# Kernel tuning notes

Hardware: AMD Instinct MI355X
Metric: run time of the kernel (lower is better)

The kernel has to match this reference:

```python
import jax, jax.numpy as jnp
import numpy as np

N_NODES = 100000
N_EDGES = 1600000
N_KEEP = 1280000  # int(N_EDGES * (1 - thr_a)), thr_a = 0.2
F_IN = 128
F_OUT = 128


def setup_inputs() -> dict:
    key = jax.random.key(0)
    ks = jax.random.split(key, 7)
    x = jax.random.normal(ks[0], (N_NODES, F_IN), dtype=jnp.float32)
    W = jax.random.normal(ks[1], (F_OUT, F_IN), dtype=jnp.float32) * (1.0 / np.sqrt(F_IN))
    bias = jax.random.normal(ks[2], (F_OUT,), dtype=jnp.float32)
    edge_src = jax.random.randint(ks[3], (N_EDGES,), 0, N_NODES, dtype=jnp.int32)
    edge_dst = jax.random.randint(ks[4], (N_EDGES,), 0, N_NODES, dtype=jnp.int32)
    edge_weight = jax.random.uniform(ks[5], (N_EDGES,), dtype=jnp.float32)
    idx_keep = jax.random.randint(ks[6], (N_KEEP,), 0, N_EDGES, dtype=jnp.int32)
    return {"x": x, "W": W, "bias": bias, "edge_src": edge_src,
            "edge_dst": edge_dst, "edge_weight": edge_weight, "idx_keep": idx_keep}


def reference(x, W, bias, edge_src, edge_dst, edge_weight, idx_keep):
    # Linear transform (pyg GCNConv lin has bias=False): h = x @ W.T  -> [N, F_out]
    h = jnp.einsum('nf,of->no', x, W)
    # Edge pruning: keep a random subset of edges (scheme_a='keep')
    src = edge_src[idx_keep]          # [M_keep]
    dst = edge_dst[idx_keep]          # [M_keep]
    ew = edge_weight[idx_keep]        # [M_keep]
    # propagate: message_j = h[src] * ew ; scatter-add into dst
    msg = h[src] * ew[:, None]        # [M_keep, F_out]
    out = jax.ops.segment_sum(msg, dst, num_segments=N_NODES)
    # GCNConv separate bias
    out = out + bias
    return out
```

## Files before the change

### kernel.cpp

```cpp
#include <hip/hip_runtime.h>

#define F 128
#define LDS_STRIDE 136
#define BUCKET 40

#define NPART 64
#define PCAP 22000
#define BIN_CAP 80
#define BIN_STRIDE 81
#define PA_CHUNK 2048
#define PB_CHUNK 1024
#define PB_CHUNKS 22

typedef __attribute__((ext_vector_type(8))) short short8;
typedef __attribute__((ext_vector_type(4))) float floatx4;
typedef __attribute__((ext_vector_type(4))) float f32x4;

__device__ __forceinline__ unsigned short f32_to_bf16(float x) {
    unsigned u = __float_as_uint(x);
    unsigned r = u + 0x7FFFu + ((u >> 16) & 1u);
    return (unsigned short)(r >> 16);
}


__global__ __launch_bounds__(256, 2) void gemm_and_partition(
    const float4* __restrict__ x4, const float4* __restrict__ W4,
    unsigned short* __restrict__ h2,
    int* __restrict__ cnt, int n_nodes,
    const int* __restrict__ idx_keep, const int* __restrict__ edge_dst,
    unsigned* __restrict__ pair_buf, int* __restrict__ pair_cnt,
    int m, int npp, int n_gemm_tiles, int n_part_chunks)
{
    __shared__ __align__(16) char smem[2 * 128 * LDS_STRIDE * 2];
    const int tid = threadIdx.x;
    const int bid = blockIdx.x;

    for (int i = bid * 256 + tid; i < n_nodes; i += gridDim.x * 256)
        cnt[i] = 0;

    const int r = bid % 9, c = bid / 9;

    if (r < 5) {
        const int tile = c * 5 + r;
        if (tile >= n_gemm_tiles) return;
        short* xs  = (short*)smem;
        short* wls = xs + 128 * LDS_STRIDE;
        const int node0 = tile * 128;

        for (int i = tid; i < 128 * 32; i += 256) {
            int row = i >> 5, c4 = i & 31;
            float4 v = W4[i];
            ushort4 b;
            b.x = f32_to_bf16(v.x); b.y = f32_to_bf16(v.y);
            b.z = f32_to_bf16(v.z); b.w = f32_to_bf16(v.w);
            *(ushort4*)&wls[row * LDS_STRIDE + c4 * 4] = b;
        }
        for (int i = tid; i < 128 * 32; i += 256) {
            int row = i >> 5, c4 = i & 31;
            int n = node0 + row;
            f32x4 v = (n < n_nodes)
                          ? __builtin_nontemporal_load((const f32x4*)&x4[(size_t)n * 32 + c4])
                          : (f32x4){0.f, 0.f, 0.f, 0.f};
            ushort4 b;
            b.x = f32_to_bf16(v[0]); b.y = f32_to_bf16(v[1]);
            b.z = f32_to_bf16(v[2]); b.w = f32_to_bf16(v[3]);
            *(ushort4*)&xs[row * LDS_STRIDE + c4 * 4] = b;
        }
        __syncthreads();

        const int wave = tid >> 6, lane = tid & 63;
        const int row16 = lane & 15, quad = lane >> 4;
        const int wrow0 = wave * 32;

        floatx4 acc[2][8];
        #pragma unroll
        for (int rr = 0; rr < 2; ++rr)
            #pragma unroll
            for (int cc = 0; cc < 8; ++cc)
                acc[rr][cc] = (floatx4){0.f, 0.f, 0.f, 0.f};

        #pragma unroll
        for (int s = 0; s < 4; ++s) {
            const int koff = s * 32 + quad * 8;
            short8 a[2];
            #pragma unroll
            for (int rr = 0; rr < 2; ++rr)
                a[rr] = *(const short8*)&xs[(wrow0 + rr * 16 + row16) * LDS_STRIDE + koff];
            #pragma unroll
            for (int cc = 0; cc < 8; ++cc) {
                short8 b = *(const short8*)&wls[(cc * 16 + row16) * LDS_STRIDE + koff];
                acc[0][cc] = __builtin_amdgcn_mfma_f32_16x16x32_bf16(a[0], b, acc[0][cc], 0, 0, 0);
                acc[1][cc] = __builtin_amdgcn_mfma_f32_16x16x32_bf16(a[1], b, acc[1][cc], 0, 0, 0);
            }
        }

        #pragma unroll
        for (int rr = 0; rr < 2; ++rr) {
            #pragma unroll
            for (int reg = 0; reg < 4; ++reg) {
                int n = node0 + wrow0 + rr * 16 + quad * 4 + reg;
                if (n < n_nodes) {
                    uint4 v;
                    v.x = (unsigned)f32_to_bf16(acc[rr][0][reg]) | ((unsigned)f32_to_bf16(acc[rr][1][reg]) << 16);
                    v.y = (unsigned)f32_to_bf16(acc[rr][2][reg]) | ((unsigned)f32_to_bf16(acc[rr][3][reg]) << 16);
                    v.z = (unsigned)f32_to_bf16(acc[rr][4][reg]) | ((unsigned)f32_to_bf16(acc[rr][5][reg]) << 16);
                    v.w = (unsigned)f32_to_bf16(acc[rr][6][reg]) | ((unsigned)f32_to_bf16(acc[rr][7][reg]) << 16);
                    *(uint4*)&h2[(size_t)n * F + row16 * 8] = v;
                }
            }
        }
    } else {
        const int chunk = c * 4 + (r - 5);
        if (chunk >= n_part_chunks) return;
        unsigned (*bins)[BIN_STRIDE] = (unsigned (*)[BIN_STRIDE])smem;
        int* bcnt  = (int*)(smem + NPART * BIN_STRIDE * 4);
        int* bbase = bcnt + NPART;

        for (int i = tid; i < NPART; i += 256) bcnt[i] = 0;
        __syncthreads();

        const int e0 = chunk * PA_CHUNK;
        #pragma unroll
        for (int k = 0; k < 2; ++k) {
            const int e_lin = e0 + (k * 256 + tid) * 4;
            int kes[4]; int nv = 0;
            if (e_lin + 3 < m) {
                int4 kv = *(const int4*)&idx_keep[e_lin];
                kes[0] = kv.x; kes[1] = kv.y; kes[2] = kv.z; kes[3] = kv.w; nv = 4;
            } else {
                for (int q = 0; q < 4; ++q)
                    if (e_lin + q < m) { kes[nv++] = idx_keep[e_lin + q]; }
            }
            int ds[4];
            for (int q = 0; q < nv; ++q) ds[q] = edge_dst[kes[q]];
            for (int q = 0; q < nv; ++q) {
                int d = ds[q];
                int p = d / npp;
                int dl = d - p * npp;
                unsigned entry = ((unsigned)dl << 21) | (unsigned)kes[q];
                int pos = atomicAdd(&bcnt[p], 1);
                if (pos < BIN_CAP) {
                    bins[p][pos] = entry;
                } else {
                    int g = atomicAdd(&pair_cnt[p], 1);
                    if (g < PCAP) pair_buf[(size_t)p * PCAP + g] = entry;
                }
            }
        }
        __syncthreads();

        for (int i = tid; i < NPART; i += 256) {
            int cc = min(bcnt[i], BIN_CAP);
            bbase[i] = atomicAdd(&pair_cnt[i], cc);
        }
        __syncthreads();

        const int wave = tid >> 6, lane = tid & 63;
        for (int b = wave; b < NPART; b += 4) {
            int cc = min(bcnt[b], BIN_CAP);
            int base = bbase[b];
            for (int j = lane; j < cc; j += 64)
                if (base + j < PCAP)
                    pair_buf[(size_t)b * PCAP + base + j] = bins[b][j];
        }
    }
}

__global__ __launch_bounds__(256) void fill_scatter(const unsigned* __restrict__ pair_buf,
                                                    const int* __restrict__ pair_cnt,
                                                    const int* __restrict__ edge_src,
                                                    const float* __restrict__ edge_weight,
                                                    int* __restrict__ cnt,
                                                    unsigned* __restrict__ perm,
                                                    int npp) {
    const int p = blockIdx.x % NPART;
    const int chunk = blockIdx.x / NPART;
    const int n = min(pair_cnt[p], PCAP);
    const int i0 = chunk * PB_CHUNK;
    if (i0 >= n) return;

    unsigned e[4]; int idx[4];
    #pragma unroll
    for (int k = 0; k < 4; ++k) {
        idx[k] = i0 + k * 256 + threadIdx.x;
        e[k] = (idx[k] < n) ? pair_buf[(size_t)p * PCAP + idx[k]] : 0u;
    }
    int s[4]; float w[4];
    #pragma unroll
    for (int k = 0; k < 4; ++k) {
        int ke = (int)(e[k] & 0x1FFFFFu);
        s[k] = edge_src[ke];
        w[k] = edge_weight[ke];
    }
    #pragma unroll
    for (int k = 0; k < 4; ++k) {
        if (idx[k] < n) {
            int d = p * npp + (int)(e[k] >> 21);
            unsigned w15 = (unsigned)__float2int_rn(w[k] * 32767.0f);
            int pos = atomicAdd(&cnt[d], 1);
            if (pos < BUCKET)
                perm[d * BUCKET + pos] = ((unsigned)s[k] << 15) | w15;
        }
    }
}

__global__ __launch_bounds__(256) void pull_wave(const unsigned* __restrict__ h4,
                                                 const int* __restrict__ cnt,
                                                 const unsigned* __restrict__ perm,
                                                 const float* __restrict__ bias,
                                                 float* __restrict__ out,
                                                 int n_nodes) {
    const int node = blockIdx.x * 4 + (threadIdx.x >> 6);
    const int lane = threadIdx.x & 63;
    if (node >= n_nodes) return;

    const int deg = min(cnt[node], BUCKET);

    int s = 0; float w = 0.0f;
    if (lane < deg) {
        unsigned entry = perm[node * BUCKET + lane];
        s = (int)(entry >> 15);
        w = (float)(entry & 0x7FFFu) * (1.0f / 32767.0f);
    }

    float acc0 = 0.0f, acc1 = 0.0f;
    for (int j = 0; j < deg; j += 4) {
        int sj[4]; float wj[4];
        #pragma unroll
        for (int q = 0; q < 4; ++q) {
            int jj = j + q;
            int take = (jj < deg) ? jj : 0;
            sj[q] = __shfl(s, take, 64);
            float t = __shfl(w, take, 64);
            wj[q] = (jj < deg) ? t : 0.0f;
        }
        unsigned hv[4];
        #pragma unroll
        for (int q = 0; q < 4; ++q)
            hv[q] = h4[(size_t)sj[q] * 64 + lane];
        #pragma unroll
        for (int q = 0; q < 4; ++q) {
            acc0 += __uint_as_float(hv[q] << 16) * wj[q];
            acc1 += __uint_as_float(hv[q] & 0xFFFF0000u) * wj[q];
        }
    }

    const int feat0 = 32 * (lane & 3) + (lane >> 2);
    const int feat1 = feat0 + 16;
    __builtin_nontemporal_store(acc0 + bias[feat0], &out[(size_t)node * F + feat0]);
    __builtin_nontemporal_store(acc1 + bias[feat1], &out[(size_t)node * F + feat1]);
}

extern "C" void kernel_launch(void* const* d_in, const int* in_sizes, int n_in,
                              void* d_out, int out_size, void* d_ws, size_t ws_size,
                              hipStream_t stream) {
    const float* x           = (const float*)d_in[0];
    const float* W           = (const float*)d_in[1];
    const float* bias        = (const float*)d_in[2];
    const int*   edge_src    = (const int*)d_in[3];
    const int*   edge_dst    = (const int*)d_in[4];
    const float* edge_weight = (const float*)d_in[5];
    const int*   idx_keep    = (const int*)d_in[6];
    float* out = (float*)d_out;

    const int n_nodes = in_sizes[0] / F;
    const int m_keep  = in_sizes[6];
    const int npp = (n_nodes + NPART - 1) / NPART;

    char* ws = (char*)d_ws;
    unsigned short* h2 = (unsigned short*)ws;
    size_t off = (size_t)n_nodes * F * 2;
    int* cnt = (int*)(ws + off);          off += (size_t)n_nodes * 4;
    int* pair_cnt = (int*)(ws + off);     off += 1024;
    unsigned* pair_buf = (unsigned*)(ws + off); off += (size_t)NPART * PCAP * 4;
    unsigned* perm = (unsigned*)(ws + off);

    const int n_gemm_tiles  = (n_nodes + 127) / 128;
    const int n_part_chunks = (m_keep + PA_CHUNK - 1) / PA_CHUNK;
    const int gens = max((n_gemm_tiles + 4) / 5, (n_part_chunks + 3) / 4);
    const int grid = 9 * gens;

    hipMemsetAsync(pair_cnt, 0, 1024, stream);

    gemm_and_partition<<<grid, 256, 0, stream>>>(
        (const float4*)x, (const float4*)W, h2, cnt, n_nodes,
        idx_keep, edge_dst, pair_buf, pair_cnt,
        m_keep, npp, n_gemm_tiles, n_part_chunks);

    fill_scatter<<<NPART * PB_CHUNKS, 256, 0, stream>>>(
        pair_buf, pair_cnt, edge_src, edge_weight, cnt, perm, npp);

    pull_wave<<<(n_nodes + 3) / 4, 256, 0, stream>>>(
        (const unsigned*)h2, cnt, perm, bias, out, n_nodes);
}
```

Baseline: 264.3 us.

## Bin edges by edge index first to localize edge array gathers

The partition pass no longer gathers edge_dst randomly. It bins kept edge indices by their high bits, so the new resolve_bin kernel reads edge_src, edge_dst and edge_weight from a localized range of edge ids. resolve_bin then re-bins by destination partition into separate dl/payload buffers, and fill_scatter only scatters the precomputed payloads. This aims to replace random gathers over the edge arrays with cache-friendly ones, at the cost of an extra kernel launch and an extra round of intermediate buffer traffic. pair1 aliases perm in the workspace, which is only safe because perm is written after pair1 is consumed.

```diff
diff --git a/kernel.cpp b/kernel.cpp
--- a/kernel.cpp
+++ b/kernel.cpp
@@ -5,11 +5,16 @@
 #define BUCKET 40
 
 #define NPART 64
+#define KE_SHIFT 15
+#define PCAP1 27500
 #define PCAP 22000
 #define BIN_CAP 80
 #define BIN_STRIDE 81
+#define BIN2_CAP 48
+#define BIN2_STRIDE 49
 #define PA_CHUNK 2048
 #define PB_CHUNK 1024
+#define PB1_CHUNKS 27
 #define PB_CHUNKS 22
 
 typedef __attribute__((ext_vector_type(8))) short short8;
@@ -23,13 +28,13 @@
 }
 
 
-__global__ __launch_bounds__(256, 2) void gemm_and_partition(
+__global__ __launch_bounds__(256, 2) void gemm_and_keybin(
     const float4* __restrict__ x4, const float4* __restrict__ W4,
     unsigned short* __restrict__ h2,
     int* __restrict__ cnt, int n_nodes,
-    const int* __restrict__ idx_keep, const int* __restrict__ edge_dst,
-    unsigned* __restrict__ pair_buf, int* __restrict__ pair_cnt,
-    int m, int npp, int n_gemm_tiles, int n_part_chunks)
+    const int* __restrict__ idx_keep,
+    unsigned* __restrict__ pair1, int* __restrict__ pair_cnt1,
+    int m, int n_gemm_tiles, int n_part_chunks)
 {
     __shared__ __align__(16) char smem[2 * 128 * LDS_STRIDE * 2];
     const int tid = threadIdx.x;
@@ -131,19 +136,15 @@
                 for (int q = 0; q < 4; ++q)
                     if (e_lin + q < m) { kes[nv++] = idx_keep[e_lin + q]; }
             }
-            int ds[4];
-            for (int q = 0; q < nv; ++q) ds[q] = edge_dst[kes[q]];
             for (int q = 0; q < nv; ++q) {
-                int d = ds[q];
-                int p = d / npp;
-                int dl = d - p * npp;
-                unsigned entry = ((unsigned)dl << 21) | (unsigned)kes[q];
+                unsigned ke = (unsigned)kes[q];
+                int p = (int)(ke >> KE_SHIFT);
                 int pos = atomicAdd(&bcnt[p], 1);
                 if (pos < BIN_CAP) {
-                    bins[p][pos] = entry;
+                    bins[p][pos] = ke;
                 } else {
-                    int g = atomicAdd(&pair_cnt[p], 1);
-                    if (g < PCAP) pair_buf[(size_t)p * PCAP + g] = entry;
+                    int g = atomicAdd(&pair_cnt1[p], 1);
+                    if (g < PCAP1) pair1[(size_t)p * PCAP1 + g] = ke;
                 }
             }
         }
@@ -151,7 +152,7 @@
 
         for (int i = tid; i < NPART; i += 256) {
             int cc = min(bcnt[i], BIN_CAP);
-            bbase[i] = atomicAdd(&pair_cnt[i], cc);
+            bbase[i] = atomicAdd(&pair_cnt1[i], cc);
         }
         __syncthreads();
 
@@ -160,46 +161,111 @@
             int cc = min(bcnt[b], BIN_CAP);
             int base = bbase[b];
             for (int j = lane; j < cc; j += 64)
-                if (base + j < PCAP)
-                    pair_buf[(size_t)b * PCAP + base + j] = bins[b][j];
-        }
-    }
-}
-
-__global__ __launch_bounds__(256) void fill_scatter(const unsigned* __restrict__ pair_buf,
-                                                    const int* __restrict__ pair_cnt,
-                                                    const int* __restrict__ edge_src,
-                                                    const float* __restrict__ edge_weight,
-                                                    int* __restrict__ cnt,
-                                                    unsigned* __restrict__ perm,
-                                                    int npp) {
+                if (base + j < PCAP1)
+                    pair1[(size_t)b * PCAP1 + base + j] = bins[b][j];
+        }
+    }
+}
+
+__global__ __launch_bounds__(256) void resolve_bin(
+    const unsigned* __restrict__ pair1, const int* __restrict__ pair_cnt1,
+    const int* __restrict__ edge_src, const int* __restrict__ edge_dst,
+    const float* __restrict__ edge_weight,
+    unsigned short* __restrict__ bufDL, unsigned* __restrict__ bufPay,
+    int* __restrict__ pair_cnt2, int npp)
+{
+    __shared__ unsigned long long bins[NPART][BIN2_STRIDE];
+    __shared__ int bcnt[NPART];
+    __shared__ int bbase[NPART];
+    const int q = blockIdx.x % NPART;
+    const int chunk = blockIdx.x / NPART;
+    const int n = min(pair_cnt1[q], PCAP1);
+    const int i0 = chunk * PB_CHUNK;
+    if (i0 >= n) return;
+
+    const int tid = threadIdx.x;
+    for (int i = tid; i < NPART; i += 256) bcnt[i] = 0;
+    __syncthreads();
+
+    unsigned kes[4]; int idx[4];
+    #pragma unroll
+    for (int k = 0; k < 4; ++k) {
+        idx[k] = i0 + k * 256 + tid;
+        kes[k] = (idx[k] < n) ? pair1[(size_t)q * PCAP1 + idx[k]] : (unsigned)(q << KE_SHIFT);
+    }
+    int s[4], d[4]; float w[4];
+    #pragma unroll
+    for (int k = 0; k < 4; ++k) {
+        s[k] = edge_src[kes[k]];
+        d[k] = edge_dst[kes[k]];
+        w[k] = edge_weight[kes[k]];
+    }
+    #pragma unroll
+    for (int k = 0; k < 4; ++k) {
+        if (idx[k] < n) {
+            int p = d[k] / npp;
+            int dl = d[k] - p * npp;
+            unsigned w15 = (unsigned)__float2int_rn(w[k] * 32767.0f);
+            unsigned pay = ((unsigned)s[k] << 15) | w15;
+            unsigned long long entry = ((unsigned long long)dl << 32) | pay;
+            int pos = atomicAdd(&bcnt[p], 1);
+            if (pos < BIN2_CAP) {
+                bins[p][pos] = entry;
+            } else {
+                int g = atomicAdd(&pair_cnt2[p], 1);
+                if (g < PCAP) {
+                    bufDL[(size_t)p * PCAP + g] = (unsigned short)dl;
+                    bufPay[(size_t)p * PCAP + g] = pay;
+                }
+            }
+        }
+    }
+    __syncthreads();
+
+    for (int i = tid; i < NPART; i += 256) {
+        int cc = min(bcnt[i], BIN2_CAP);
+        bbase[i] = atomicAdd(&pair_cnt2[i], cc);
+    }
+    __syncthreads();
+
+    const int wave = tid >> 6, lane = tid & 63;
+    for (int b = wave; b < NPART; b += 4) {
+        int cc = min(bcnt[b], BIN2_CAP);
+        int base = bbase[b];
+        for (int j = lane; j < cc; j += 64)
+            if (base + j < PCAP) {
+                unsigned long long e = bins[b][j];
+                bufDL[(size_t)b * PCAP + base + j] = (unsigned short)(e >> 32);
+                bufPay[(size_t)b * PCAP + base + j] = (unsigned)e;
+            }
+    }
+}
+
+__global__ __launch_bounds__(256) void fill_scatter(
+    const unsigned short* __restrict__ bufDL, const unsigned* __restrict__ bufPay,
+    const int* __restrict__ pair_cnt2,
+    int* __restrict__ cnt, unsigned* __restrict__ perm, int npp)
+{
     const int p = blockIdx.x % NPART;
     const int chunk = blockIdx.x / NPART;
-    const int n = min(pair_cnt[p], PCAP);
+    const int n = min(pair_cnt2[p], PCAP);
     const int i0 = chunk * PB_CHUNK;
     if (i0 >= n) return;
 
-    unsigned e[4]; int idx[4];
+    int idx[4]; int dl[4]; unsigned pay[4];
     #pragma unroll
     for (int k = 0; k < 4; ++k) {
         idx[k] = i0 + k * 256 + threadIdx.x;
-        e[k] = (idx[k] < n) ? pair_buf[(size_t)p * PCAP + idx[k]] : 0u;
-    }
-    int s[4]; float w[4];
-    #pragma unroll
-    for (int k = 0; k < 4; ++k) {
-        int ke = (int)(e[k] & 0x1FFFFFu);
-        s[k] = edge_src[ke];
-        w[k] = edge_weight[ke];
+        int safe = (idx[k] < n) ? idx[k] : i0;
+        dl[k] = bufDL[(size_t)p * PCAP + safe];
+        pay[k] = bufPay[(size_t)p * PCAP + safe];
     }
     #pragma unroll
     for (int k = 0; k < 4; ++k) {
         if (idx[k] < n) {
-            int d = p * npp + (int)(e[k] >> 21);
-            unsigned w15 = (unsigned)__float2int_rn(w[k] * 32767.0f);
+            int d = p * npp + dl[k];
             int pos = atomicAdd(&cnt[d], 1);
-            if (pos < BUCKET)
-                perm[d * BUCKET + pos] = ((unsigned)s[k] << 15) | w15;
+            if (pos < BUCKET) perm[d * BUCKET + pos] = pay[k];
         }
     }
 }
@@ -270,25 +336,31 @@
     char* ws = (char*)d_ws;
     unsigned short* h2 = (unsigned short*)ws;
     size_t off = (size_t)n_nodes * F * 2;
-    int* cnt = (int*)(ws + off);          off += (size_t)n_nodes * 4;
-    int* pair_cnt = (int*)(ws + off);     off += 1024;
-    unsigned* pair_buf = (unsigned*)(ws + off); off += (size_t)NPART * PCAP * 4;
-    unsigned* perm = (unsigned*)(ws + off);
+    int* cnt = (int*)(ws + off);              off += (size_t)n_nodes * 4;
+    int* pair_cnt1 = (int*)(ws + off);
+    int* pair_cnt2 = (int*)(ws + off + 1024); off += 2048;
+    unsigned short* bufDL = (unsigned short*)(ws + off); off += (size_t)NPART * PCAP * 2;
+    unsigned* bufPay = (unsigned*)(ws + off); off += (size_t)NPART * PCAP * 4;
+    unsigned* pair1 = (unsigned*)(ws + off);
+    unsigned* perm  = (unsigned*)(ws + off);
 
     const int n_gemm_tiles  = (n_nodes + 127) / 128;
     const int n_part_chunks = (m_keep + PA_CHUNK - 1) / PA_CHUNK;
     const int gens = max((n_gemm_tiles + 4) / 5, (n_part_chunks + 3) / 4);
     const int grid = 9 * gens;
 
-    hipMemsetAsync(pair_cnt, 0, 1024, stream);
-
-    gemm_and_partition<<<grid, 256, 0, stream>>>(
+    hipMemsetAsync(pair_cnt1, 0, 2048, stream);
+
+    gemm_and_keybin<<<grid, 256, 0, stream>>>(
         (const float4*)x, (const float4*)W, h2, cnt, n_nodes,
-        idx_keep, edge_dst, pair_buf, pair_cnt,
-        m_keep, npp, n_gemm_tiles, n_part_chunks);
+        idx_keep, pair1, pair_cnt1, m_keep, n_gemm_tiles, n_part_chunks);
+
+    resolve_bin<<<NPART * PB1_CHUNKS, 256, 0, stream>>>(
+        pair1, pair_cnt1, edge_src, edge_dst, edge_weight,
+        bufDL, bufPay, pair_cnt2, npp);
 
     fill_scatter<<<NPART * PB_CHUNKS, 256, 0, stream>>>(
-        pair_buf, pair_cnt, edge_src, edge_weight, cnt, perm, npp);
+        bufDL, bufPay, pair_cnt2, cnt, perm, npp);
 
     pull_wave<<<(n_nodes + 3) / 4, 256, 0, stream>>>(
         (const unsigned*)h2, cnt, perm, bias, out, n_nodes);
```

New measurement: 275.4 us. +4.2%, slower.
